# Optimization experiments

Hardware: AMD Instinct MI355X
Metric: run time of the kernel (lower is better)

Reference implementation:

```python
import jax, jax.numpy as jnp
import numpy as np

N, E, F, H = 100000, 1000000, 128, 64
BN_EPS = 1e-3  # keras BatchNormalization default epsilon


def setup_inputs() -> dict:
    key = jax.random.key(0)
    k_x, k_src, k_dst, k_w = jax.random.split(key, 4)
    node_features = jax.random.normal(k_x, (N, F), dtype=jnp.float32)
    # Ensure every node appears at least once as a source so that
    # deg**-0.5 is finite (the original code implicitly assumes this).
    src = jnp.concatenate([
        jnp.arange(N, dtype=jnp.int32),
        jax.random.randint(k_src, (E - N,), 0, N, dtype=jnp.int32),
    ])
    dst = jax.random.randint(k_dst, (E,), 0, N, dtype=jnp.int32)
    edge_index = jnp.stack([src, dst], axis=1)  # [E, 2]
    # glorot_uniform for kernel
    limit = np.sqrt(6.0 / (F + H)).astype(np.float32)
    W = jax.random.uniform(k_w, (F, H), dtype=jnp.float32, minval=-limit, maxval=limit)
    b = jnp.zeros((H,), dtype=jnp.float32)
    bn_gamma = jnp.ones((H,), dtype=jnp.float32)
    bn_beta = jnp.zeros((H,), dtype=jnp.float32)
    bn_mean = jnp.zeros((H,), dtype=jnp.float32)
    bn_var = jnp.ones((H,), dtype=jnp.float32)
    return dict(node_features=node_features, W=W, b=b, bn_gamma=bn_gamma,
                bn_beta=bn_beta, bn_mean=bn_mean, bn_var=bn_var,
                edge_index=edge_index)


def reference(node_features, W, b, bn_gamma, bn_beta, bn_mean, bn_var, edge_index):
    n = node_features.shape[0]
    src = edge_index[:, 0]
    dst = edge_index[:, 1]
    # Dense transform; dropout is identity in inference (training=False).
    h = node_features @ W + b  # [N, H]
    # Out-degree per node (segments keyed by src, matching the TF code).
    deg = jax.ops.segment_sum(jnp.ones(src.shape, h.dtype), src, num_segments=n)  # [N]
    inv_sqrt_deg = deg ** -0.5
    # Per-edge symmetric-style scaling: deg(src)^-0.5 * deg(dst)^-0.5 * h[dst]
    edge_scale = inv_sqrt_deg[src] * inv_sqrt_deg[dst]  # [E]
    neigh = edge_scale[:, None] * h[dst]  # [E, H]
    agg = 0.5 * jax.ops.segment_sum(neigh, src, num_segments=n)  # [N, H]
    # Self term: segment_mean of deg(src) * h[src] over src segments.
    self_term = deg[src][:, None] * h[src]  # [E, H]
    self_sum = jax.ops.segment_sum(self_term, src, num_segments=n)  # [N, H]
    self_mean = self_sum / jnp.maximum(deg, 1.0)[:, None]
    agg = agg + 0.5 * self_mean
    # BatchNormalization in inference mode.
    out = (agg - bn_mean) * (bn_gamma * jax.lax.rsqrt(bn_var + BN_EPS)) + bn_beta
    return out
```

## Files before the change

### kernel.cpp

```cpp
#include <hip/hip_runtime.h>

#define BN_EPS 0.001f
#define CAP 32

typedef __attribute__((ext_vector_type(8))) short bf16x8;
typedef __attribute__((ext_vector_type(4))) float f32x4;

__device__ __forceinline__ unsigned short f2bf(float f) {
  unsigned u = __float_as_uint(f);
  u += 0x7fffu + ((u >> 16) & 1u);
  return (unsigned short)(u >> 16);
}

__global__ __launch_bounds__(256) void k_fused(
    const float* __restrict__ X, const float* __restrict__ W,
    const float* __restrict__ B, unsigned short* __restrict__ hb, int N,
    const int2* __restrict__ ei, int* __restrict__ cnt,
    int* __restrict__ ell, int E, int Gs) {
  __shared__ float WtF[4096];

  int tid = threadIdx.x;

  if ((int)blockIdx.x < Gs) {
    int e0 = (blockIdx.x * 256 + tid) * 4;
    if (e0 + 3 < E) {
      const int4* p = (const int4*)ei;
      int4 a = p[e0 >> 1];
      int4 b = p[(e0 >> 1) + 1];
      int p0 = atomicAdd(&cnt[a.x], 1);
      int p1 = atomicAdd(&cnt[a.z], 1);
      int p2 = atomicAdd(&cnt[b.x], 1);
      int p3 = atomicAdd(&cnt[b.z], 1);
      if (p0 < CAP) ell[(size_t)a.x * CAP + p0] = a.y;
      if (p1 < CAP) ell[(size_t)a.z * CAP + p1] = a.w;
      if (p2 < CAP) ell[(size_t)b.x * CAP + p2] = b.y;
      if (p3 < CAP) ell[(size_t)b.z * CAP + p3] = b.w;
    } else {
      for (int e = e0; e < E; ++e) {
        int2 sd = ei[e];
        int pos = atomicAdd(&cnt[sd.x], 1);
        if (pos < CAP) ell[(size_t)sd.x * CAP + pos] = sd.y;
      }
    }
    return;
  }

  int tile = blockIdx.x - Gs;

  char* Wt = (char*)WtF;
  const float4* W4 = (const float4*)W;
  for (int i = tid; i < 2048; i += 256) {
    float4 v = W4[i];
    int k = i >> 4;
    int col0 = (i & 15) << 2;
    int kb2 = k << 1;
    *(unsigned short*)(Wt + (((col0 + 0) << 8) | (kb2 ^ (((col0 + 0) & 7) << 4)))) = f2bf(v.x);
    *(unsigned short*)(Wt + (((col0 + 1) << 8) | (kb2 ^ (((col0 + 1) & 7) << 4)))) = f2bf(v.y);
    *(unsigned short*)(Wt + (((col0 + 2) << 8) | (kb2 ^ (((col0 + 2) & 7) << 4)))) = f2bf(v.z);
    *(unsigned short*)(Wt + (((col0 + 3) << 8) | (kb2 ^ (((col0 + 3) & 7) << 4)))) = f2bf(v.w);
  }
  __syncthreads();

  int lane = tid & 63;
  int w = tid >> 6;
  int l15 = lane & 15;
  int lk = lane >> 4;

  int row0 = tile * 64;
  int rA = row0 + w * 16 + l15;
  bool rowok = rA < N;
  const float* xp = X + (size_t)rA * 128 + (lk << 3);

  f32x4 acc[4];
  #pragma unroll
  for (int n = 0; n < 4; ++n) {
    float bv = B[(n << 4) + l15];
    acc[n] = (f32x4){bv, bv, bv, bv};
  }

  #pragma unroll
  for (int kb = 0; kb < 4; ++kb) {
    bf16x8 af = {0, 0, 0, 0, 0, 0, 0, 0};
    if (rowok) {
      float4 x0 = *(const float4*)(xp + kb * 32);
      float4 x1 = *(const float4*)(xp + kb * 32 + 4);
      af[0] = (short)f2bf(x0.x); af[1] = (short)f2bf(x0.y);
      af[2] = (short)f2bf(x0.z); af[3] = (short)f2bf(x0.w);
      af[4] = (short)f2bf(x1.x); af[5] = (short)f2bf(x1.y);
      af[6] = (short)f2bf(x1.z); af[7] = (short)f2bf(x1.w);
    }
    int kbyte = (kb << 6) | (lk << 4);
    #pragma unroll
    for (int n = 0; n < 4; ++n) {
      int col = (n << 4) + l15;
      bf16x8 bfr = *(const bf16x8*)(Wt + ((col << 8) | (kbyte ^ ((col & 7) << 4))));
      acc[n] = __builtin_amdgcn_mfma_f32_16x16x32_bf16(af, bfr, acc[n], 0, 0, 0);
    }
  }

  int rbase = row0 + w * 16 + (lk << 2);
  #pragma unroll
  for (int n = 0; n < 4; ++n) {
    #pragma unroll
    for (int q = 0; q < 4; ++q) {
      int row = rbase + q;
      if (row < N) hb[(size_t)row * 64 + (n << 4) + l15] = f2bf(acc[n][q]);
    }
  }
}

__global__ __launch_bounds__(256) void k_aggfinal(const int* __restrict__ cnt,
                                                  const int* __restrict__ ell,
                                                  const unsigned int* __restrict__ hb32,
                                                  const float* __restrict__ gamma,
                                                  const float* __restrict__ beta,
                                                  const float* __restrict__ mean,
                                                  const float* __restrict__ var,
                                                  float* __restrict__ out, int N) {
  int wave = threadIdx.x >> 6;
  int lane = threadIdx.x & 63;
  int sub  = lane >> 5;
  int fp   = lane & 31;
  int node = blockIdx.x * 8 + wave * 2 + sub;
  if (node >= N) return;

  int d_raw = ell[(size_t)node * CAP + fp];
  int c0 = cnt[node];
  int dm = ((unsigned)d_raw < (unsigned)N) ? d_raw : 0;
  int c = (c0 < CAP) ? c0 : CAP;
  float s = 0.f;
  if (fp < c) s = rsqrtf((float)cnt[dm]);

  int base = sub << 5;

  float ax = 0.f, ay = 0.f;
  int q = 0;
  for (; q + 4 <= c; q += 4) {
    int d0 = __shfl(dm, base + q);
    int d1 = __shfl(dm, base + q + 1);
    int d2 = __shfl(dm, base + q + 2);
    int d3 = __shfl(dm, base + q + 3);
    float s0 = __shfl(s, base + q);
    float s1 = __shfl(s, base + q + 1);
    float s2 = __shfl(s, base + q + 2);
    float s3 = __shfl(s, base + q + 3);
    unsigned u0 = hb32[(size_t)d0 * 32 + fp];
    unsigned u1 = hb32[(size_t)d1 * 32 + fp];
    unsigned u2 = hb32[(size_t)d2 * 32 + fp];
    unsigned u3 = hb32[(size_t)d3 * 32 + fp];
    ax = fmaf(s0, __uint_as_float(u0 << 16), ax);
    ay = fmaf(s0, __uint_as_float(u0 & 0xffff0000u), ay);
    ax = fmaf(s1, __uint_as_float(u1 << 16), ax);
    ay = fmaf(s1, __uint_as_float(u1 & 0xffff0000u), ay);
    ax = fmaf(s2, __uint_as_float(u2 << 16), ax);
    ay = fmaf(s2, __uint_as_float(u2 & 0xffff0000u), ay);
    ax = fmaf(s3, __uint_as_float(u3 << 16), ax);
    ay = fmaf(s3, __uint_as_float(u3 & 0xffff0000u), ay);
  }
  for (; q < c; ++q) {
    int dq = __shfl(dm, base + q);
    float sq = __shfl(s, base + q);
    unsigned u = hb32[(size_t)dq * 32 + fp];
    ax = fmaf(sq, __uint_as_float(u << 16), ax);
    ay = fmaf(sq, __uint_as_float(u & 0xffff0000u), ay);
  }

  int j = fp * 2;
  unsigned us = hb32[(size_t)node * 32 + fp];
  float hx = __uint_as_float(us << 16);
  float hy = __uint_as_float(us & 0xffff0000u);

  float degf = (float)c0;
  float isd_n = rsqrtf((float)((c0 > 0) ? c0 : 1));
  float rx = 0.5f * (isd_n * ax + degf * hx);
  float ry = 0.5f * (isd_n * ay + degf * hy);

  float2 gm = *(const float2*)&gamma[j];
  float2 bt = *(const float2*)&beta[j];
  float2 mn = *(const float2*)&mean[j];
  float2 vr = *(const float2*)&var[j];
  float2 o;
  o.x = (rx - mn.x) * (gm.x * rsqrtf(vr.x + BN_EPS)) + bt.x;
  o.y = (ry - mn.y) * (gm.y * rsqrtf(vr.y + BN_EPS)) + bt.y;
  *(float2*)&out[(size_t)node * 64 + j] = o;
}

extern "C" void kernel_launch(void* const* d_in, const int* in_sizes, int n_in,
                              void* d_out, int out_size, void* d_ws, size_t ws_size,
                              hipStream_t stream) {
  const float* X     = (const float*)d_in[0];
  const float* W     = (const float*)d_in[1];
  const float* B     = (const float*)d_in[2];
  const float* gamma = (const float*)d_in[3];
  const float* beta  = (const float*)d_in[4];
  const float* mean  = (const float*)d_in[5];
  const float* var   = (const float*)d_in[6];
  const int2*  ei    = (const int2*)d_in[7];

  int N = in_sizes[0] / 128;
  int E = in_sizes[7] / 2;

  unsigned short* hb  = (unsigned short*)d_ws;
  int*            ell = (int*)(hb + (size_t)N * 64);
  int*            cnt = ell + (size_t)N * CAP;
  float*          out = (float*)d_out;

  hipMemsetAsync(cnt, 0, (size_t)N * sizeof(int), stream);

  int Gs = (E + 1023) / 1024;
  int Gg = (N + 63) / 64;
  k_fused<<<Gs + Gg, 256, 0, stream>>>(X, W, B, hb, N, ei, cnt, ell, E, Gs);

  k_aggfinal<<<(N + 7) / 8, 256, 0, stream>>>(cnt, ell, (const unsigned int*)hb,
                                              gamma, beta, mean, var, out, N);
}
```

Baseline: 213.4 us.

## Prescale neighbor features by inverse sqrt degree and interleave scatter with GEMM blocks

Adds a pass that writes a copy of h already multiplied by each node's deg^-0.5 in bf16. The aggregation kernel then sums the gathered rows directly, dropping the per-edge degree lookup and shuffle of scales, and unrolls the gather by 8 for more loads in flight. The fused kernel now interleaves edge-scatter blocks (one edge per thread) with GEMM tile blocks in a 5:2 pattern so both kinds run side by side. The cost is an extra kernel launch, an extra N×64 bf16 buffer round trip, and a second bf16 rounding after the scaling. If the workspace is too small it falls back to the old gather path.

```diff
diff --git a/kernel.cpp b/kernel.cpp
--- a/kernel.cpp
+++ b/kernel.cpp
@@ -11,41 +11,37 @@
   u += 0x7fffu + ((u >> 16) & 1u);
   return (unsigned short)(u >> 16);
 }
+__device__ __forceinline__ unsigned scale2(unsigned u, float s) {
+  float lo = __uint_as_float(u << 16) * s;
+  float hi = __uint_as_float(u & 0xffff0000u) * s;
+  return (((unsigned)f2bf(hi)) << 16) | (unsigned)f2bf(lo);
+}
 
 __global__ __launch_bounds__(256) void k_fused(
     const float* __restrict__ X, const float* __restrict__ W,
-    const float* __restrict__ B, unsigned short* __restrict__ hb, int N,
+    const float* __restrict__ B, unsigned short* __restrict__ hb, int N, int Gg,
     const int2* __restrict__ ei, int* __restrict__ cnt,
     int* __restrict__ ell, int E, int Gs) {
   __shared__ float WtF[4096];
 
+  int g = blockIdx.x / 7;
+  int r = blockIdx.x % 7;
   int tid = threadIdx.x;
 
-  if ((int)blockIdx.x < Gs) {
-    int e0 = (blockIdx.x * 256 + tid) * 4;
-    if (e0 + 3 < E) {
-      const int4* p = (const int4*)ei;
-      int4 a = p[e0 >> 1];
-      int4 b = p[(e0 >> 1) + 1];
-      int p0 = atomicAdd(&cnt[a.x], 1);
-      int p1 = atomicAdd(&cnt[a.z], 1);
-      int p2 = atomicAdd(&cnt[b.x], 1);
-      int p3 = atomicAdd(&cnt[b.z], 1);
-      if (p0 < CAP) ell[(size_t)a.x * CAP + p0] = a.y;
-      if (p1 < CAP) ell[(size_t)a.z * CAP + p1] = a.w;
-      if (p2 < CAP) ell[(size_t)b.x * CAP + p2] = b.y;
-      if (p3 < CAP) ell[(size_t)b.z * CAP + p3] = b.w;
-    } else {
-      for (int e = e0; e < E; ++e) {
-        int2 sd = ei[e];
-        int pos = atomicAdd(&cnt[sd.x], 1);
-        if (pos < CAP) ell[(size_t)sd.x * CAP + pos] = sd.y;
-      }
+  if (r >= 2) {
+    int chunk = g * 5 + (r - 2);
+    if (chunk >= Gs) return;
+    int e = chunk * 256 + tid;
+    if (e < E) {
+      int2 sd = ei[e];
+      int pos = atomicAdd(&cnt[sd.x], 1);
+      if (pos < CAP) ell[(size_t)sd.x * CAP + pos] = sd.y;
     }
     return;
   }
 
-  int tile = blockIdx.x - Gs;
+  int tile = g * 2 + r;
+  if (tile >= Gg) return;
 
   char* Wt = (char*)WtF;
   const float4* W4 = (const float4*)W;
@@ -109,14 +105,30 @@
   }
 }
 
-__global__ __launch_bounds__(256) void k_aggfinal(const int* __restrict__ cnt,
-                                                  const int* __restrict__ ell,
-                                                  const unsigned int* __restrict__ hb32,
-                                                  const float* __restrict__ gamma,
-                                                  const float* __restrict__ beta,
-                                                  const float* __restrict__ mean,
-                                                  const float* __restrict__ var,
-                                                  float* __restrict__ out, int N) {
+__global__ __launch_bounds__(256) void k_scale(const unsigned int* __restrict__ hb32,
+                                               const int* __restrict__ cnt,
+                                               unsigned int* __restrict__ hbs32, int N) {
+  int t = blockIdx.x * 256 + threadIdx.x;
+  int node = t >> 3;
+  int q = t & 7;
+  if (node >= N) return;
+  int c = cnt[node];
+  float s = rsqrtf((float)((c > 0) ? c : 1));
+  uint4 v = ((const uint4*)(hb32 + (size_t)node * 32))[q];
+  v.x = scale2(v.x, s); v.y = scale2(v.y, s);
+  v.z = scale2(v.z, s); v.w = scale2(v.w, s);
+  ((uint4*)(hbs32 + (size_t)node * 32))[q] = v;
+}
+
+__global__ __launch_bounds__(256) void k_aggfinal_s(const int* __restrict__ cnt,
+                                                    const int* __restrict__ ell,
+                                                    const unsigned int* __restrict__ hb32,
+                                                    const unsigned int* __restrict__ hbs32,
+                                                    const float* __restrict__ gamma,
+                                                    const float* __restrict__ beta,
+                                                    const float* __restrict__ mean,
+                                                    const float* __restrict__ var,
+                                                    float* __restrict__ out, int N) {
   int wave = threadIdx.x >> 6;
   int lane = threadIdx.x & 63;
   int sub  = lane >> 5;
@@ -126,11 +138,92 @@
 
   int d_raw = ell[(size_t)node * CAP + fp];
   int c0 = cnt[node];
+  unsigned us = hb32[(size_t)node * 32 + fp];
+  int dm = ((unsigned)d_raw < (unsigned)N) ? d_raw : 0;
+  int c = (c0 < CAP) ? c0 : CAP;
+  int base = sub << 5;
+
+  float ax = 0.f, ay = 0.f;
+  int q = 0;
+  for (; q + 8 <= c; q += 8) {
+    int d[8];
+    #pragma unroll
+    for (int i = 0; i < 8; ++i) d[i] = __shfl(dm, base + q + i);
+    unsigned u[8];
+    #pragma unroll
+    for (int i = 0; i < 8; ++i) u[i] = hbs32[(size_t)d[i] * 32 + fp];
+    #pragma unroll
+    for (int i = 0; i < 8; ++i) {
+      ax += __uint_as_float(u[i] << 16);
+      ay += __uint_as_float(u[i] & 0xffff0000u);
+    }
+  }
+  if (q + 4 <= c) {
+    int d0 = __shfl(dm, base + q);
+    int d1 = __shfl(dm, base + q + 1);
+    int d2 = __shfl(dm, base + q + 2);
+    int d3 = __shfl(dm, base + q + 3);
+    unsigned u0 = hbs32[(size_t)d0 * 32 + fp];
+    unsigned u1 = hbs32[(size_t)d1 * 32 + fp];
+    unsigned u2 = hbs32[(size_t)d2 * 32 + fp];
+    unsigned u3 = hbs32[(size_t)d3 * 32 + fp];
+    ax += __uint_as_float(u0 << 16);
+    ay += __uint_as_float(u0 & 0xffff0000u);
+    ax += __uint_as_float(u1 << 16);
+    ay += __uint_as_float(u1 & 0xffff0000u);
+    ax += __uint_as_float(u2 << 16);
+    ay += __uint_as_float(u2 & 0xffff0000u);
+    ax += __uint_as_float(u3 << 16);
+    ay += __uint_as_float(u3 & 0xffff0000u);
+    q += 4;
+  }
+  for (; q < c; ++q) {
+    int dq = __shfl(dm, base + q);
+    unsigned u = hbs32[(size_t)dq * 32 + fp];
+    ax += __uint_as_float(u << 16);
+    ay += __uint_as_float(u & 0xffff0000u);
+  }
+
+  int j = fp * 2;
+  float hx = __uint_as_float(us << 16);
+  float hy = __uint_as_float(us & 0xffff0000u);
+
+  float degf = (float)c0;
+  float isd_n = rsqrtf((float)((c0 > 0) ? c0 : 1));
+  float rx = 0.5f * (isd_n * ax + degf * hx);
+  float ry = 0.5f * (isd_n * ay + degf * hy);
+
+  float2 gm = *(const float2*)&gamma[j];
+  float2 bt = *(const float2*)&beta[j];
+  float2 mn = *(const float2*)&mean[j];
+  float2 vr = *(const float2*)&var[j];
+  float2 o;
+  o.x = (rx - mn.x) * (gm.x * rsqrtf(vr.x + BN_EPS)) + bt.x;
+  o.y = (ry - mn.y) * (gm.y * rsqrtf(vr.y + BN_EPS)) + bt.y;
+  *(float2*)&out[(size_t)node * 64 + j] = o;
+}
+
+__global__ __launch_bounds__(256) void k_aggfinal_g(const int* __restrict__ cnt,
+                                                    const int* __restrict__ ell,
+                                                    const unsigned int* __restrict__ hb32,
+                                                    const float* __restrict__ gamma,
+                                                    const float* __restrict__ beta,
+                                                    const float* __restrict__ mean,
+                                                    const float* __restrict__ var,
+                                                    float* __restrict__ out, int N) {
+  int wave = threadIdx.x >> 6;
+  int lane = threadIdx.x & 63;
+  int sub  = lane >> 5;
+  int fp   = lane & 31;
+  int node = blockIdx.x * 8 + wave * 2 + sub;
+  if (node >= N) return;
+
+  int d_raw = ell[(size_t)node * CAP + fp];
+  int c0 = cnt[node];
   int dm = ((unsigned)d_raw < (unsigned)N) ? d_raw : 0;
   int c = (c0 < CAP) ? c0 : CAP;
   float s = 0.f;
   if (fp < c) s = rsqrtf((float)cnt[dm]);
-
   int base = sub << 5;
 
   float ax = 0.f, ay = 0.f;
@@ -199,18 +292,38 @@
 
   int N = in_sizes[0] / 128;
   int E = in_sizes[7] / 2;
-
-  unsigned short* hb  = (unsigned short*)d_ws;
-  int*            ell = (int*)(hb + (size_t)N * 64);
-  int*            cnt = ell + (size_t)N * CAP;
-  float*          out = (float*)d_out;
-
-  hipMemsetAsync(cnt, 0, (size_t)N * sizeof(int), stream);
-
-  int Gs = (E + 1023) / 1024;
+  float* out = (float*)d_out;
+
+  size_t hb_elems = (size_t)N * 64;
+  size_t need_hbs = hb_elems * 2 * 2 + (size_t)N * CAP * 4 + (size_t)N * 4;
+
+  int Gs = (E + 255) / 256;
   int Gg = (N + 63) / 64;
-  k_fused<<<Gs + Gg, 256, 0, stream>>>(X, W, B, hb, N, ei, cnt, ell, E, Gs);
-
-  k_aggfinal<<<(N + 7) / 8, 256, 0, stream>>>(cnt, ell, (const unsigned int*)hb,
-                                              gamma, beta, mean, var, out, N);
-}
+  int g7 = (Gg + 1) / 2;
+  int g5 = (Gs + 4) / 5;
+  int groups = (g7 > g5) ? g7 : g5;
+
+  if (ws_size >= need_hbs) {
+    unsigned short* hb  = (unsigned short*)d_ws;
+    unsigned short* hbs = hb + hb_elems;
+    int*            ell = (int*)(hbs + hb_elems);
+    int*            cnt = ell + (size_t)N * CAP;
+
+    hipMemsetAsync(cnt, 0, (size_t)N * sizeof(int), stream);
+    k_fused<<<groups * 7, 256, 0, stream>>>(X, W, B, hb, N, Gg, ei, cnt, ell, E, Gs);
+    k_scale<<<(N * 8 + 255) / 256, 256, 0, stream>>>((const unsigned int*)hb, cnt,
+                                                     (unsigned int*)hbs, N);
+    k_aggfinal_s<<<(N + 7) / 8, 256, 0, stream>>>(cnt, ell, (const unsigned int*)hb,
+                                                  (const unsigned int*)hbs,
+                                                  gamma, beta, mean, var, out, N);
+  } else {
+    unsigned short* hb  = (unsigned short*)d_ws;
+    int*            ell = (int*)(hb + hb_elems);
+    int*            cnt = ell + (size_t)N * CAP;
+
+    hipMemsetAsync(cnt, 0, (size_t)N * sizeof(int), stream);
+    k_fused<<<groups * 7, 256, 0, stream>>>(X, W, B, hb, N, Gg, ei, cnt, ell, E, Gs);
+    k_aggfinal_g<<<(N + 7) / 8, 256, 0, stream>>>(cnt, ell, (const unsigned int*)hb,
+                                                  gamma, beta, mean, var, out, N);
+  }
+}
```

Result: faster. 200.6 us (-6.0%).

## Partition edge scatter by source range, transpose ELL layout, stage neighbor lists in LDS

Applied to the files above, without the earlier changes.

The edge scatter is split into 8 source-node partitions. Each edge segment is read by 8 blocks, and each block only handles sources in its range, so atomics and writes stay within a smaller region. The ELL table becomes slot-major (pos*N+node), which the aggregation kernel loads coalesced into LDS for 64 nodes per block. Aggregation now recomputes neighbor degree scaling per lane from cnt and unrolls the gathers by 8 for more memory-level parallelism. The cost is that the edge list is read 8 times, and each lane does extra cnt gathers.

```diff
diff --git a/kernel.cpp b/kernel.cpp
--- a/kernel.cpp
+++ b/kernel.cpp
@@ -2,6 +2,8 @@
 
 #define BN_EPS 0.001f
 #define CAP 32
+#define NPART 8
+#define SEGE 4096
 
 typedef __attribute__((ext_vector_type(8))) short bf16x8;
 typedef __attribute__((ext_vector_type(4))) float f32x4;
@@ -14,38 +16,50 @@
 
 __global__ __launch_bounds__(256) void k_fused(
     const float* __restrict__ X, const float* __restrict__ W,
-    const float* __restrict__ B, unsigned short* __restrict__ hb, int N,
+    const float* __restrict__ B, unsigned short* __restrict__ hb, int N, int Gg,
     const int2* __restrict__ ei, int* __restrict__ cnt,
-    int* __restrict__ ell, int E, int Gs) {
+    int* __restrict__ ell_t, int E) {
   __shared__ float WtF[4096];
 
+  int bid = blockIdx.x;
   int tid = threadIdx.x;
-
-  if ((int)blockIdx.x < Gs) {
-    int e0 = (blockIdx.x * 256 + tid) * 4;
-    if (e0 + 3 < E) {
-      const int4* p = (const int4*)ei;
-      int4 a = p[e0 >> 1];
-      int4 b = p[(e0 >> 1) + 1];
-      int p0 = atomicAdd(&cnt[a.x], 1);
-      int p1 = atomicAdd(&cnt[a.z], 1);
-      int p2 = atomicAdd(&cnt[b.x], 1);
-      int p3 = atomicAdd(&cnt[b.z], 1);
-      if (p0 < CAP) ell[(size_t)a.x * CAP + p0] = a.y;
-      if (p1 < CAP) ell[(size_t)a.z * CAP + p1] = a.w;
-      if (p2 < CAP) ell[(size_t)b.x * CAP + p2] = b.y;
-      if (p3 < CAP) ell[(size_t)b.z * CAP + p3] = b.w;
-    } else {
-      for (int e = e0; e < E; ++e) {
-        int2 sd = ei[e];
+  int gid = bid >> 4;
+  int slot = bid & 15;
+
+  if (slot < 8) {
+    int p = slot;
+    int lo = (int)((long long)p * N / NPART);
+    int hi = (int)((long long)(p + 1) * N / NPART);
+    const int4* e4 = (const int4*)ei;
+    int n4 = E >> 1;
+    int base4 = gid * (SEGE / 2);
+    #pragma unroll
+    for (int i = 0; i < 8; ++i) {
+      int q = base4 + i * 256 + tid;
+      if (q < n4) {
+        int4 v = e4[q];
+        if (v.x >= lo && v.x < hi) {
+          int pos = atomicAdd(&cnt[v.x], 1);
+          if (pos < CAP) ell_t[(size_t)pos * N + v.x] = v.y;
+        }
+        if (v.z >= lo && v.z < hi) {
+          int pos = atomicAdd(&cnt[v.z], 1);
+          if (pos < CAP) ell_t[(size_t)pos * N + v.z] = v.w;
+        }
+      }
+    }
+    if ((E & 1) && gid == 0 && tid == 0) {
+      int2 sd = ei[E - 1];
+      if (sd.x >= lo && sd.x < hi) {
         int pos = atomicAdd(&cnt[sd.x], 1);
-        if (pos < CAP) ell[(size_t)sd.x * CAP + pos] = sd.y;
+        if (pos < CAP) ell_t[(size_t)pos * N + sd.x] = sd.y;
       }
     }
     return;
   }
 
-  int tile = blockIdx.x - Gs;
+  int tile = gid * 8 + (slot - 8);
+  if (tile >= Gg) return;
 
   char* Wt = (char*)WtF;
   const float4* W4 = (const float4*)W;
@@ -109,80 +123,119 @@
   }
 }
 
-__global__ __launch_bounds__(256) void k_aggfinal(const int* __restrict__ cnt,
-                                                  const int* __restrict__ ell,
-                                                  const unsigned int* __restrict__ hb32,
-                                                  const float* __restrict__ gamma,
-                                                  const float* __restrict__ beta,
-                                                  const float* __restrict__ mean,
-                                                  const float* __restrict__ var,
-                                                  float* __restrict__ out, int N) {
-  int wave = threadIdx.x >> 6;
-  int lane = threadIdx.x & 63;
-  int sub  = lane >> 5;
-  int fp   = lane & 31;
-  int node = blockIdx.x * 8 + wave * 2 + sub;
-  if (node >= N) return;
-
-  int d_raw = ell[(size_t)node * CAP + fp];
-  int c0 = cnt[node];
-  int dm = ((unsigned)d_raw < (unsigned)N) ? d_raw : 0;
-  int c = (c0 < CAP) ? c0 : CAP;
-  float s = 0.f;
-  if (fp < c) s = rsqrtf((float)cnt[dm]);
-
-  int base = sub << 5;
-
-  float ax = 0.f, ay = 0.f;
-  int q = 0;
-  for (; q + 4 <= c; q += 4) {
-    int d0 = __shfl(dm, base + q);
-    int d1 = __shfl(dm, base + q + 1);
-    int d2 = __shfl(dm, base + q + 2);
-    int d3 = __shfl(dm, base + q + 3);
-    float s0 = __shfl(s, base + q);
-    float s1 = __shfl(s, base + q + 1);
-    float s2 = __shfl(s, base + q + 2);
-    float s3 = __shfl(s, base + q + 3);
-    unsigned u0 = hb32[(size_t)d0 * 32 + fp];
-    unsigned u1 = hb32[(size_t)d1 * 32 + fp];
-    unsigned u2 = hb32[(size_t)d2 * 32 + fp];
-    unsigned u3 = hb32[(size_t)d3 * 32 + fp];
-    ax = fmaf(s0, __uint_as_float(u0 << 16), ax);
-    ay = fmaf(s0, __uint_as_float(u0 & 0xffff0000u), ay);
-    ax = fmaf(s1, __uint_as_float(u1 << 16), ax);
-    ay = fmaf(s1, __uint_as_float(u1 & 0xffff0000u), ay);
-    ax = fmaf(s2, __uint_as_float(u2 << 16), ax);
-    ay = fmaf(s2, __uint_as_float(u2 & 0xffff0000u), ay);
-    ax = fmaf(s3, __uint_as_float(u3 << 16), ax);
-    ay = fmaf(s3, __uint_as_float(u3 & 0xffff0000u), ay);
-  }
-  for (; q < c; ++q) {
-    int dq = __shfl(dm, base + q);
-    float sq = __shfl(s, base + q);
-    unsigned u = hb32[(size_t)dq * 32 + fp];
-    ax = fmaf(sq, __uint_as_float(u << 16), ax);
-    ay = fmaf(sq, __uint_as_float(u & 0xffff0000u), ay);
-  }
-
-  int j = fp * 2;
-  unsigned us = hb32[(size_t)node * 32 + fp];
-  float hx = __uint_as_float(us << 16);
-  float hy = __uint_as_float(us & 0xffff0000u);
-
-  float degf = (float)c0;
-  float isd_n = rsqrtf((float)((c0 > 0) ? c0 : 1));
-  float rx = 0.5f * (isd_n * ax + degf * hx);
-  float ry = 0.5f * (isd_n * ay + degf * hy);
-
-  float2 gm = *(const float2*)&gamma[j];
-  float2 bt = *(const float2*)&beta[j];
-  float2 mn = *(const float2*)&mean[j];
-  float2 vr = *(const float2*)&var[j];
-  float2 o;
-  o.x = (rx - mn.x) * (gm.x * rsqrtf(vr.x + BN_EPS)) + bt.x;
-  o.y = (ry - mn.y) * (gm.y * rsqrtf(vr.y + BN_EPS)) + bt.y;
-  *(float2*)&out[(size_t)node * 64 + j] = o;
+__global__ __launch_bounds__(256) void k_agg(const int* __restrict__ cnt,
+                                             const int* __restrict__ ell_t,
+                                             const unsigned int* __restrict__ hb32,
+                                             const float* __restrict__ gamma,
+                                             const float* __restrict__ beta,
+                                             const float* __restrict__ mean,
+                                             const float* __restrict__ var,
+                                             float* __restrict__ out, int N) {
+  __shared__ int lds_dst[CAP * 64];
+  __shared__ int lds_cnt[64];
+
+  int tid = threadIdx.x;
+  int node0 = blockIdx.x * 64;
+
+  if (tid < 64) {
+    int n = node0 + tid;
+    lds_cnt[tid] = (n < N) ? cnt[n] : 0;
+  }
+  for (int i = tid; i < CAP * 64; i += 256) {
+    int j = i & 63;
+    int p = i >> 6;
+    int n = node0 + j;
+    lds_dst[i] = (n < N) ? ell_t[(size_t)p * N + n] : 0;
+  }
+  __syncthreads();
+
+  int hw = tid >> 5;
+  int fp = tid & 31;
+
+  float2 gm = *(const float2*)&gamma[fp * 2];
+  float2 bt = *(const float2*)&beta[fp * 2];
+  float2 mn = *(const float2*)&mean[fp * 2];
+  float2 vr = *(const float2*)&var[fp * 2];
+  float gsx = gm.x * rsqrtf(vr.x + BN_EPS);
+  float gsy = gm.y * rsqrtf(vr.y + BN_EPS);
+
+  #pragma unroll
+  for (int t = 0; t < 8; ++t) {
+    int j = hw * 8 + t;
+    int node = node0 + j;
+    if (node >= N) continue;
+    int c0 = lds_cnt[j];
+    int c = (c0 < CAP) ? c0 : CAP;
+    unsigned us = hb32[(size_t)node * 32 + fp];
+
+    float ax = 0.f, ay = 0.f;
+    int q = 0;
+    for (; q + 8 <= c; q += 8) {
+      int d[8];
+      #pragma unroll
+      for (int i = 0; i < 8; ++i) {
+        int dr = lds_dst[(q + i) * 64 + j];
+        d[i] = ((unsigned)dr < (unsigned)N) ? dr : 0;
+      }
+      int cc[8];
+      #pragma unroll
+      for (int i = 0; i < 8; ++i) cc[i] = cnt[d[i]];
+      unsigned u[8];
+      #pragma unroll
+      for (int i = 0; i < 8; ++i) u[i] = hb32[(size_t)d[i] * 32 + fp];
+      #pragma unroll
+      for (int i = 0; i < 8; ++i) {
+        float s = rsqrtf((float)((cc[i] > 0) ? cc[i] : 1));
+        ax = fmaf(s, __uint_as_float(u[i] << 16), ax);
+        ay = fmaf(s, __uint_as_float(u[i] & 0xffff0000u), ay);
+      }
+    }
+    if (q + 4 <= c) {
+      int d0 = lds_dst[(q + 0) * 64 + j]; d0 = ((unsigned)d0 < (unsigned)N) ? d0 : 0;
+      int d1 = lds_dst[(q + 1) * 64 + j]; d1 = ((unsigned)d1 < (unsigned)N) ? d1 : 0;
+      int d2 = lds_dst[(q + 2) * 64 + j]; d2 = ((unsigned)d2 < (unsigned)N) ? d2 : 0;
+      int d3 = lds_dst[(q + 3) * 64 + j]; d3 = ((unsigned)d3 < (unsigned)N) ? d3 : 0;
+      int c0_ = cnt[d0], c1_ = cnt[d1], c2_ = cnt[d2], c3_ = cnt[d3];
+      unsigned u0 = hb32[(size_t)d0 * 32 + fp];
+      unsigned u1 = hb32[(size_t)d1 * 32 + fp];
+      unsigned u2 = hb32[(size_t)d2 * 32 + fp];
+      unsigned u3 = hb32[(size_t)d3 * 32 + fp];
+      float s0 = rsqrtf((float)((c0_ > 0) ? c0_ : 1));
+      float s1 = rsqrtf((float)((c1_ > 0) ? c1_ : 1));
+      float s2 = rsqrtf((float)((c2_ > 0) ? c2_ : 1));
+      float s3 = rsqrtf((float)((c3_ > 0) ? c3_ : 1));
+      ax = fmaf(s0, __uint_as_float(u0 << 16), ax);
+      ay = fmaf(s0, __uint_as_float(u0 & 0xffff0000u), ay);
+      ax = fmaf(s1, __uint_as_float(u1 << 16), ax);
+      ay = fmaf(s1, __uint_as_float(u1 & 0xffff0000u), ay);
+      ax = fmaf(s2, __uint_as_float(u2 << 16), ax);
+      ay = fmaf(s2, __uint_as_float(u2 & 0xffff0000u), ay);
+      ax = fmaf(s3, __uint_as_float(u3 << 16), ax);
+      ay = fmaf(s3, __uint_as_float(u3 & 0xffff0000u), ay);
+      q += 4;
+    }
+    for (; q < c; ++q) {
+      int dq = lds_dst[q * 64 + j];
+      dq = ((unsigned)dq < (unsigned)N) ? dq : 0;
+      int cq = cnt[dq];
+      unsigned u = hb32[(size_t)dq * 32 + fp];
+      float sq = rsqrtf((float)((cq > 0) ? cq : 1));
+      ax = fmaf(sq, __uint_as_float(u << 16), ax);
+      ay = fmaf(sq, __uint_as_float(u & 0xffff0000u), ay);
+    }
+
+    float hx = __uint_as_float(us << 16);
+    float hy = __uint_as_float(us & 0xffff0000u);
+    float degf = (float)c0;
+    float isd_n = rsqrtf((float)((c0 > 0) ? c0 : 1));
+    float rx = 0.5f * (isd_n * ax + degf * hx);
+    float ry = 0.5f * (isd_n * ay + degf * hy);
+
+    float2 o;
+    o.x = (rx - mn.x) * gsx + bt.x;
+    o.y = (ry - mn.y) * gsy + bt.y;
+    *(float2*)&out[(size_t)node * 64 + fp * 2] = o;
+  }
 }
 
 extern "C" void kernel_launch(void* const* d_in, const int* in_sizes, int n_in,
@@ -199,18 +252,21 @@
 
   int N = in_sizes[0] / 128;
   int E = in_sizes[7] / 2;
+  float* out = (float*)d_out;
 
   unsigned short* hb  = (unsigned short*)d_ws;
   int*            ell = (int*)(hb + (size_t)N * 64);
   int*            cnt = ell + (size_t)N * CAP;
-  float*          out = (float*)d_out;
-
-  hipMemsetAsync(cnt, 0, (size_t)N * sizeof(int), stream);
-
-  int Gs = (E + 1023) / 1024;
+
+  (void)hipMemsetAsync(cnt, 0, (size_t)N * sizeof(int), stream);
+
   int Gg = (N + 63) / 64;
-  k_fused<<<Gs + Gg, 256, 0, stream>>>(X, W, B, hb, N, ei, cnt, ell, E, Gs);
-
-  k_aggfinal<<<(N + 7) / 8, 256, 0, stream>>>(cnt, ell, (const unsigned int*)hb,
-                                              gamma, beta, mean, var, out, N);
-}
+  int nsegs = (E + SEGE - 1) / SEGE;
+  int ngg = (Gg + 7) / 8;
+  int ngroups = (nsegs > ngg) ? nsegs : ngg;
+  k_fused<<<ngroups * 16, 256, 0, stream>>>(X, W, B, hb, N, Gg, ei, cnt, ell, E);
+
+  int Ga = (N + 63) / 64;
+  k_agg<<<Ga, 256, 0, stream>>>(cnt, ell, (const unsigned int*)hb,
+                                gamma, beta, mean, var, out, N);
+}
```

Result: faster. 178.8 us (-16.2%).
